# Kernel optimization log

Measured on AMD Instinct MI355X. Metric: run time of the kernel, lower is better.

Reference implementation:

```python
import jax, jax.numpy as jnp
import numpy as np

D_MODEL = 1024
N_HEADS = 16
HEAD_DIM = D_MODEL // N_HEADS


def setup_inputs() -> dict:
    key = jax.random.key(0)
    ks = jax.random.split(key, 5)
    B, T = 4, 4096
    x = jax.random.normal(ks[0], (B, T, D_MODEL), dtype=jnp.float32)
    s = 1.0 / np.sqrt(D_MODEL)
    Wqkv = jax.random.normal(ks[1], (D_MODEL, 3 * D_MODEL), dtype=jnp.float32) * s
    bqkv = jnp.zeros((3 * D_MODEL,), dtype=jnp.float32)
    Wout = jax.random.normal(ks[2], (D_MODEL, D_MODEL), dtype=jnp.float32) * s
    bout = jnp.zeros((D_MODEL,), dtype=jnp.float32)
    return {"x": x, "Wqkv": Wqkv, "bqkv": bqkv, "Wout": Wout, "bout": bout}


def _feature_map(x):
    # elu(x) + 1  (strictly positive feature map)
    return jax.nn.elu(x) + 1.0


def reference(x, Wqkv, bqkv, Wout, bout):
    B, T, C = x.shape
    H, D = N_HEADS, HEAD_DIM
    qkv = x @ Wqkv + bqkv                      # [B,T,3C]
    qkv = qkv.reshape(B, T, 3, H, D)
    qkv = jnp.transpose(qkv, (2, 0, 3, 1, 4))  # [3,B,H,T,D]
    q, k, v = qkv[0], qkv[1], qkv[2]
    scale = D ** 0.25
    q_m = _feature_map(q / scale)
    k_m = _feature_map(k / scale)
    kv = jnp.einsum('bhtd,bhtm->bhdm', k_m, v)     # [B,H,D,D]
    out = jnp.einsum('bhtd,bhdm->bhtm', q_m, kv)   # [B,H,T,D]
    z = q_m.sum(axis=-1, keepdims=True)            # note: sum over feature dim (as in source)
    out = out / (z + 1e-6)
    out = jnp.transpose(out, (0, 2, 1, 3)).reshape(B, T, C)
    return out @ Wout + bout
```

## Files before the change

kernel.cpp:

```cpp
#include <hip/hip_runtime.h>
#include <hip/hip_bf16.h>
#include <math.h>

#define B_ 4
#define T_ 4096
#define H_ 16
#define D_ 64
#define C_ 1024
#define BT_ (B_*T_)

using short8  = __attribute__((ext_vector_type(8))) short;
using floatx4 = __attribute__((ext_vector_type(4))) float;

__device__ __forceinline__ float feature_map(float x) {
    return x > 0.0f ? x + 1.0f : __expf(x);
}
__device__ __forceinline__ unsigned short f2bf(float x) {
    union { __hip_bfloat16 b; unsigned short u; } c;
    c.b = __float2bfloat16(x);
    return c.u;
}
__device__ __forceinline__ float bf2f(unsigned short u) {
    union { unsigned int u; float f; } c;
    c.u = (unsigned)u << 16;
    return c.f;
}
__device__ __forceinline__ void async16(const void* g, void* l) {
    __builtin_amdgcn_global_load_lds(
        (const __attribute__((address_space(1))) void*)g,
        (__attribute__((address_space(3))) void*)l, 16, 0, 0);
}

__global__ __launch_bounds__(256)
void convert_x_kernel(const float4* __restrict__ x, ushort* __restrict__ xb)
{
    const size_t i = (size_t)blockIdx.x * 256 + threadIdx.x;
    const float4 v = x[i];
    *reinterpret_cast<ushort4*>(&xb[i * 4]) =
        make_ushort4(f2bf(v.x), f2bf(v.y), f2bf(v.z), f2bf(v.w));
}

__global__ __launch_bounds__(256)
void transpose_bf16_kernel(const float* __restrict__ W, ushort* __restrict__ WT,
                           int K, int N)
{
    __shared__ float t[32][33];
    const int n0 = blockIdx.x * 32, k0 = blockIdx.y * 32;
    const int r = threadIdx.x >> 5, c = threadIdx.x & 31;
    #pragma unroll
    for (int i = 0; i < 4; i++)
        t[r + 8 * i][c] = W[(size_t)(k0 + r + 8 * i) * N + n0 + c];
    __syncthreads();
    #pragma unroll
    for (int i = 0; i < 4; i++)
        WT[(size_t)(n0 + r + 8 * i) * K + k0 + c] = f2bf(t[c][r + 8 * i]);
}

#define BAR()    __builtin_amdgcn_s_barrier()
#define WAITDS() do { asm volatile("s_waitcnt lgkmcnt(0)" ::: "memory"); \
                      __builtin_amdgcn_sched_barrier(0); } while(0)
#define VM6()    do { asm volatile("s_waitcnt vmcnt(6)" ::: "memory"); \
                      __builtin_amdgcn_sched_barrier(0); } while(0)

#define LDA(slot, mf, ks, buf) \
    aR[slot][ks] = *(const short8*)(smem + (buf)*32768 + ((mf)>>2)*16384 + \
                                    aRowB + ((mf)&3)*2048 + cks##ks)
#define LDB(nf, ks, buf) \
    bR[nf][ks] = *(const short8*)(smem + 65536 + (buf)*32768 + ((nf)>>1)*16384 + \
                                  bRowB + ((nf)&1)*2048 + cks##ks)
#define LDA8(MB, BUF) do { \
    LDA(0, MB+0, 0, BUF); LDA(0, MB+0, 1, BUF); \
    LDA(1, MB+1, 0, BUF); LDA(1, MB+1, 1, BUF); \
    LDA(2, MB+2, 0, BUF); LDA(2, MB+2, 1, BUF); \
    LDA(3, MB+3, 0, BUF); LDA(3, MB+3, 1, BUF); } while(0)
#define LDB4(NF, BUF) do { \
    LDB(NF+0, 0, BUF); LDB(NF+0, 1, BUF); \
    LDB(NF+1, 0, BUF); LDB(NF+1, 1, BUF); } while(0)

#define MM(mf, nf, ks, slot) \
    acc[mf][nf] = __builtin_amdgcn_mfma_f32_16x16x32_bf16( \
        aR[slot][ks], bR[nf][ks], acc[mf][nf], 0, 0, 0)
#define MFMAQ(MB, NF) do { \
    MM(MB+0,NF+0,0,0); MM(MB+1,NF+0,0,1); MM(MB+2,NF+0,0,2); MM(MB+3,NF+0,0,3); \
    MM(MB+0,NF+1,0,0); MM(MB+1,NF+1,0,1); MM(MB+2,NF+1,0,2); MM(MB+3,NF+1,0,3); \
    MM(MB+0,NF+0,1,0); MM(MB+1,NF+0,1,1); MM(MB+2,NF+0,1,2); MM(MB+3,NF+0,1,3); \
    MM(MB+0,NF+1,1,0); MM(MB+1,NF+1,1,1); MM(MB+2,NF+1,1,2); MM(MB+3,NF+1,1,3); \
} while(0)

#define STG(SRC, OPB, h, w, buf) do { \
    async16(SRC[h][0] + (size_t)(w)*128, \
            smem + (OPB) + (buf)*32768 + (h)*16384 + wv*1024); \
    async16(SRC[h][1] + (size_t)(w)*128, \
            smem + (OPB) + (buf)*32768 + (h)*16384 + 8192 + wv*1024); \
} while(0)

template<int EPI, int NBX>
__global__ __launch_bounds__(512, 2)
void gemm256_8ph(const ushort* __restrict__ A, const ushort* __restrict__ Bm,
                 const float* __restrict__ bias,
                 ushort* __restrict__ q_out, ushort* __restrict__ kT_out,
                 ushort* __restrict__ vT_out, float* __restrict__ f_out)
{
    __shared__ __align__(16) unsigned char smem[131072];

    const int tid = threadIdx.x;
    const int wv = tid >> 6, l = tid & 63;
    const int wm = wv >> 2, wn = wv & 3;
    const int lr = l & 15, quad = l >> 4;

    int wg = blockIdx.x;
    { const int cpx = (int)gridDim.x >> 3; wg = (wg & 7) * cpx + (wg >> 3); }
    const int mb = wg / NBX, nb = wg % NBX;
    const int mBase = mb * 256, nBase = nb * 256;

    const int s0 = tid >> 3;
    const int cb = ((tid & 7) * 16) ^ ((s0 & 7) << 4);
    const char* Abyte = (const char*)(A + (size_t)mBase * C_);
    const char* Bbyte = (const char*)(Bm + (size_t)nBase * C_);
    const char* aSrc[2][2]; const char* bSrc[2][2];
    #pragma unroll
    for (int h = 0; h < 2; h++) {
        aSrc[h][0] = Abyte + (size_t)(h * 64 + s0) * 2048 + cb;
        aSrc[h][1] = Abyte + (size_t)(128 + h * 64 + s0) * 2048 + cb;
        const int bq = (s0 >> 5) * 64 + h * 32 + (s0 & 31);
        bSrc[h][0] = Bbyte + (size_t)bq * 2048 + cb;
        bSrc[h][1] = Bbyte + (size_t)(bq + 128) * 2048 + cb;
    }

    const int aRowB = (wm * 64 + lr) * 128;
    const int bRowB = (wn * 32 + lr) * 128;
    const int cks0 = (quad * 16) ^ ((lr & 7) << 4);
    const int cks1 = 64 ^ cks0;

    floatx4 acc[8][4];
    #pragma unroll
    for (int i = 0; i < 8; i++)
        #pragma unroll
        for (int j = 0; j < 4; j++) acc[i][j] = (floatx4)0.0f;
    short8 aR[4][2], bR[4][2];

    STG(aSrc,     0, 0, 0, 0);
    STG(bSrc, 65536, 0, 0, 0);
    STG(bSrc, 65536, 1, 0, 0);
    STG(aSrc,     0, 1, 0, 0);
    STG(aSrc,     0, 0, 1, 1);
    STG(bSrc, 65536, 0, 1, 1);
    STG(bSrc, 65536, 1, 1, 1);
    asm volatile("s_waitcnt vmcnt(6)" ::: "memory");
    __builtin_amdgcn_sched_barrier(0);
    BAR();

    #pragma unroll 1
    for (int it = 0; it < 8; ++it) {
        const int t1v = 2 * it + 1;
        const int t2v = (2 * it + 2) & 15;
        const int t3v = (2 * it + 3) & 15;
        LDA8(0, 0); LDB4(0, 0);
        STG(aSrc, 0, 1, t1v, 1);
        BAR(); WAITDS(); __builtin_amdgcn_s_setprio(1); MFMAQ(0, 0);
        __builtin_amdgcn_s_setprio(0); BAR();
        LDB4(2, 0);
        STG(aSrc, 0, 0, t2v, 0);
        BAR(); WAITDS(); __builtin_amdgcn_s_setprio(1); MFMAQ(0, 2);
        __builtin_amdgcn_s_setprio(0); BAR();
        LDA8(4, 0);
        STG(bSrc, 65536, 0, t2v, 0);
        BAR(); WAITDS(); __builtin_amdgcn_s_setprio(1); MFMAQ(4, 2);
        __builtin_amdgcn_s_setprio(0); BAR();
        STG(bSrc, 65536, 1, t2v, 0);
        BAR(); WAITDS(); __builtin_amdgcn_s_setprio(1); MFMAQ(4, 0);
        __builtin_amdgcn_s_setprio(0); VM6(); BAR();
        LDA8(0, 1); LDB4(0, 1);
        STG(aSrc, 0, 1, t2v, 0);
        BAR(); WAITDS(); __builtin_amdgcn_s_setprio(1); MFMAQ(0, 0);
        __builtin_amdgcn_s_setprio(0); BAR();
        LDB4(2, 1);
        STG(aSrc, 0, 0, t3v, 1);
        BAR(); WAITDS(); __builtin_amdgcn_s_setprio(1); MFMAQ(0, 2);
        __builtin_amdgcn_s_setprio(0); BAR();
        LDA8(4, 1);
        STG(bSrc, 65536, 0, t3v, 1);
        BAR(); WAITDS(); __builtin_amdgcn_s_setprio(1); MFMAQ(4, 2);
        __builtin_amdgcn_s_setprio(0); BAR();
        STG(bSrc, 65536, 1, t3v, 1);
        BAR(); WAITDS(); __builtin_amdgcn_s_setprio(1); MFMAQ(4, 0);
        __builtin_amdgcn_s_setprio(0); VM6(); BAR();
    }

    if (EPI == 0) {
        const float inv_scale = 0.35355339059327373f;
        const int seg = nBase >> 10;
        if (seg == 0) {
            #pragma unroll
            for (int nf = 0; nf < 4; nf++) {
                const int c = nBase + wn * 64 + nf * 16 + lr;
                const float bv = bias[c];
                #pragma unroll
                for (int mf = 0; mf < 8; mf++)
                    #pragma unroll
                    for (int i = 0; i < 4; i++) {
                        const int t = mBase + wm * 128 + mf * 16 + quad * 4 + i;
                        q_out[(size_t)t * C_ + c] =
                            f2bf(feature_map((acc[mf][nf][i] + bv) * inv_scale));
                    }
            }
        } else {
            ushort* dstT = (seg == 1) ? kT_out : vT_out;
            #pragma unroll
            for (int nf = 0; nf < 4; nf++) {
                const int cfull = nBase + wn * 64 + nf * 16 + lr;
                const int c = cfull & 1023;
                const float bv = bias[cfull];
                #pragma unroll
                for (int mf = 0; mf < 8; mf++) {
                    float v0 = acc[mf][nf][0] + bv, v1 = acc[mf][nf][1] + bv;
                    float v2 = acc[mf][nf][2] + bv, v3 = acc[mf][nf][3] + bv;
                    if (seg == 1) {
                        v0 = feature_map(v0 * inv_scale); v1 = feature_map(v1 * inv_scale);
                        v2 = feature_map(v2 * inv_scale); v3 = feature_map(v3 * inv_scale);
                    }
                    const int tt = mBase + wm * 128 + mf * 16 + quad * 4;
                    *(ushort4*)&dstT[(size_t)c * BT_ + tt] =
                        make_ushort4(f2bf(v0), f2bf(v1), f2bf(v2), f2bf(v3));
                }
            }
        }
    } else {
        #pragma unroll
        for (int nf = 0; nf < 4; nf++) {
            const int c = nBase + wn * 64 + nf * 16 + lr;
            const float bv = bias[c];
            #pragma unroll
            for (int mf = 0; mf < 8; mf++)
                #pragma unroll
                for (int i = 0; i < 4; i++) {
                    const int row = mBase + wm * 128 + mf * 16 + quad * 4 + i;
                    f_out[(size_t)row * C_ + c] = acc[mf][nf][i] + bv;
                }
        }
    }
    asm volatile("s_waitcnt vmcnt(0)" ::: "memory");
}

__global__ __launch_bounds__(256)
void kv_accum_kernel(const ushort* __restrict__ kmT, const ushort* __restrict__ vT,
                     float* __restrict__ kv)
{
    const int tid = threadIdx.x;
    const int w = tid >> 6, l = tid & 63;
    const int wm = w >> 1, wn = w & 1;
    const int lr = l & 15, quad = l >> 4;
    const int bh = blockIdx.y;
    const int b = bh >> 4, h = bh & 15;
    const size_t t0 = (size_t)b * T_ + (size_t)blockIdx.x * 512;

    const ushort* Ar = kmT + (size_t)(h * 64 + wm * 32 + lr) * BT_ + t0 + quad * 8;
    const ushort* Br = vT  + (size_t)(h * 64 + wn * 32 + lr) * BT_ + t0 + quad * 8;

    floatx4 acc[2][2];
    #pragma unroll
    for (int i = 0; i < 2; i++)
        #pragma unroll
        for (int j = 0; j < 2; j++) acc[i][j] = (floatx4)0.0f;

    #pragma unroll 4
    for (int tt = 0; tt < 512; tt += 32) {
        const short8 af0 = *(const short8*)&Ar[tt];
        const short8 af1 = *(const short8*)&Ar[(size_t)16 * BT_ + tt];
        const short8 bf0 = *(const short8*)&Br[tt];
        const short8 bf1 = *(const short8*)&Br[(size_t)16 * BT_ + tt];
        acc[0][0] = __builtin_amdgcn_mfma_f32_16x16x32_bf16(af0, bf0, acc[0][0], 0, 0, 0);
        acc[0][1] = __builtin_amdgcn_mfma_f32_16x16x32_bf16(af0, bf1, acc[0][1], 0, 0, 0);
        acc[1][0] = __builtin_amdgcn_mfma_f32_16x16x32_bf16(af1, bf0, acc[1][0], 0, 0, 0);
        acc[1][1] = __builtin_amdgcn_mfma_f32_16x16x32_bf16(af1, bf1, acc[1][1], 0, 0, 0);
    }

    float* kvb = kv + (size_t)bh * (D_ * D_);
    #pragma unroll
    for (int i = 0; i < 2; i++)
        #pragma unroll
        for (int j = 0; j < 2; j++)
            #pragma unroll
            for (int r = 0; r < 4; r++) {
                const int d = wm * 32 + i * 16 + quad * 4 + r;
                const int m = wn * 32 + j * 16 + lr;
                atomicAdd(&kvb[d * 64 + m], acc[i][j][r]);
            }
}

__global__ __launch_bounds__(256)
void pv_kernel(const ushort* __restrict__ qm, const float* __restrict__ kv,
               ushort* __restrict__ attn)
{
    __shared__ ushort kvs[64 * 72];
    const int tid = threadIdx.x;
    const int w = tid >> 6, l = tid & 63;
    const int lr = l & 15, quad = l >> 4;
    const int h = blockIdx.x;
    const int tBase = blockIdx.y * 256;
    const int b = tBase >> 12;

    const float* kvg = kv + ((size_t)b * H_ + h) * (D_ * D_);
    #pragma unroll
    for (int e = 0; e < 4; e++) {
        const int flat = (e * 256 + tid) * 4;
        const float4 vv = *(const float4*)&kvg[flat];
        const int d = flat >> 6, m = flat & 63;
        kvs[(m + 0) * 72 + d] = f2bf(vv.x);
        kvs[(m + 1) * 72 + d] = f2bf(vv.y);
        kvs[(m + 2) * 72 + d] = f2bf(vv.z);
        kvs[(m + 3) * 72 + d] = f2bf(vv.w);
    }
    __syncthreads();

    const int tw = tBase + w * 64;

    floatx4 acc[4][4];
    #pragma unroll
    for (int i = 0; i < 4; i++)
        #pragma unroll
        for (int j = 0; j < 4; j++) acc[i][j] = (floatx4)0.0f;

    float zp[4] = {0.0f, 0.0f, 0.0f, 0.0f};

    #pragma unroll
    for (int kk = 0; kk < 2; kk++) {
        short8 bf[4];
        #pragma unroll
        for (int tf = 0; tf < 4; tf++) {
            bf[tf] = *(const short8*)&qm[(size_t)(tw + tf * 16 + lr) * C_
                                         + h * 64 + kk * 32 + quad * 8];
            #pragma unroll
            for (int j = 0; j < 8; j++) zp[tf] += bf2f((unsigned short)bf[tf][j]);
        }
        short8 af[4];
        #pragma unroll
        for (int mf = 0; mf < 4; mf++)
            af[mf] = *(const short8*)&kvs[(mf * 16 + lr) * 72 + kk * 32 + quad * 8];
        #pragma unroll
        for (int mf = 0; mf < 4; mf++)
            #pragma unroll
            for (int tf = 0; tf < 4; tf++)
                acc[mf][tf] = __builtin_amdgcn_mfma_f32_16x16x32_bf16(
                    af[mf], bf[tf], acc[mf][tf], 0, 0, 0);
    }

    #pragma unroll
    for (int tf = 0; tf < 4; tf++) {
        zp[tf] += __shfl_xor(zp[tf], 16);
        zp[tf] += __shfl_xor(zp[tf], 32);
    }

    #pragma unroll
    for (int tf = 0; tf < 4; tf++) {
        const int t = tw + tf * 16 + lr;
        const float inv = 1.0f / (zp[tf] + 1e-6f);
        #pragma unroll
        for (int mf = 0; mf < 4; mf++) {
            const int m = mf * 16 + quad * 4;
            *(ushort4*)&attn[(size_t)t * C_ + h * 64 + m] =
                make_ushort4(f2bf(acc[mf][tf][0] * inv), f2bf(acc[mf][tf][1] * inv),
                             f2bf(acc[mf][tf][2] * inv), f2bf(acc[mf][tf][3] * inv));
        }
    }
}

extern "C" void kernel_launch(void* const* d_in, const int* in_sizes, int n_in,
                              void* d_out, int out_size, void* d_ws, size_t ws_size,
                              hipStream_t stream)
{
    const float* x    = (const float*)d_in[0];
    const float* Wqkv = (const float*)d_in[1];
    const float* bqkv = (const float*)d_in[2];
    const float* Wout = (const float*)d_in[3];
    const float* bout = (const float*)d_in[4];
    float* out = (float*)d_out;

    char* ws = (char*)d_ws;
    ushort* xb     = (ushort*)ws;
    ushort* WqkvT  = (ushort*)(ws + 33554432);
    ushort* WoutT  = (ushort*)(ws + 39845888);
    ushort* vT     = (ushort*)(ws + 41943040);
    float*  kv     = (float*) (ws + 75497472);
    ushort* attn   = (ushort*)ws;
    ushort* qm     = (ushort*)d_out;
    ushort* kmT    = (ushort*)((char*)d_out + 33554432);

    hipMemsetAsync(kv, 0, (size_t)B_ * H_ * D_ * D_ * sizeof(float), stream);

    convert_x_kernel<<<(BT_ * C_ / 4) / 256, 256, 0, stream>>>((const float4*)x, xb);
    transpose_bf16_kernel<<<dim3(3 * C_ / 32, C_ / 32), 256, 0, stream>>>(Wqkv, WqkvT, C_, 3 * C_);
    transpose_bf16_kernel<<<dim3(C_ / 32, C_ / 32), 256, 0, stream>>>(Wout, WoutT, C_, C_);

    gemm256_8ph<0, 12><<<dim3(768), 512, 0, stream>>>(
        xb, WqkvT, bqkv, qm, kmT, vT, nullptr);
    kv_accum_kernel<<<dim3(8, B_ * H_), 256, 0, stream>>>(kmT, vT, kv);
    pv_kernel<<<dim3(H_, BT_ / 256), 256, 0, stream>>>(qm, kv, attn);
    gemm256_8ph<1, 4><<<dim3(256), 512, 0, stream>>>(
        attn, WoutT, bout, nullptr, nullptr, nullptr, out);
}
```

Measured before the change: 315.2 us.

## Make QKV GEMM persistent over three tiles with cross-tile prefetch

The QKV projection GEMM now launches 256 workgroups, and each computes three 256x256 output tiles in sequence. The global-to-LDS prefetch runs across tile boundaries, so loads for the next tile's first k-steps overlap the current tile's tail. Bias values are preloaded per tile and the epilogue is factored into a helper. This removes the pipeline prologue and drain for every tile after the first, at the cost of more registers, and the epilogue stores still stall between tiles. The x-to-bf16 conversion also handles 8 elements per thread with one 16-byte store, and the kv accumulation loop is unrolled further.

```diff
diff --git a/kernel.cpp b/kernel.cpp
--- a/kernel.cpp
+++ b/kernel.cpp
@@ -30,14 +30,22 @@
         (const __attribute__((address_space(1))) void*)g,
         (__attribute__((address_space(3))) void*)l, 16, 0, 0);
 }
+__device__ __forceinline__ const char* sel3(const char* a0, const char* a1,
+                                            const char* a2, int t) {
+    return t == 0 ? a0 : (t == 1 ? a1 : a2);
+}
 
 __global__ __launch_bounds__(256)
 void convert_x_kernel(const float4* __restrict__ x, ushort* __restrict__ xb)
 {
-    const size_t i = (size_t)blockIdx.x * 256 + threadIdx.x;
-    const float4 v = x[i];
-    *reinterpret_cast<ushort4*>(&xb[i * 4]) =
-        make_ushort4(f2bf(v.x), f2bf(v.y), f2bf(v.z), f2bf(v.w));
+    const size_t i = ((size_t)blockIdx.x * 256 + threadIdx.x) * 2;
+    const float4 a = x[i], b = x[i + 1];
+    short8 r;
+    r[0] = (short)f2bf(a.x); r[1] = (short)f2bf(a.y);
+    r[2] = (short)f2bf(a.z); r[3] = (short)f2bf(a.w);
+    r[4] = (short)f2bf(b.x); r[5] = (short)f2bf(b.y);
+    r[6] = (short)f2bf(b.z); r[7] = (short)f2bf(b.w);
+    *reinterpret_cast<short8*>(&xb[i * 4]) = r;
 }
 
 __global__ __launch_bounds__(256)
@@ -87,106 +95,51 @@
     MM(MB+0,NF+1,1,0); MM(MB+1,NF+1,1,1); MM(MB+2,NF+1,1,2); MM(MB+3,NF+1,1,3); \
 } while(0)
 
-#define STG(SRC, OPB, h, w, buf) do { \
-    async16(SRC[h][0] + (size_t)(w)*128, \
-            smem + (OPB) + (buf)*32768 + (h)*16384 + wv*1024); \
-    async16(SRC[h][1] + (size_t)(w)*128, \
-            smem + (OPB) + (buf)*32768 + (h)*16384 + 8192 + wv*1024); \
+#define STGA(h, G, buf) do { int _g = (G); if (_g >= NTILE*16) _g -= NTILE*16; \
+    const char* _b = sel3(Ab0, Ab1, Ab2, _g >> 4); const int _w = (_g & 15) * 128; \
+    async16(_b + aOf##h##0 + _w, smem + (buf)*32768 + (h)*16384 + wv*1024); \
+    async16(_b + aOf##h##1 + _w, smem + (buf)*32768 + (h)*16384 + 8192 + wv*1024); \
 } while(0)
-
-template<int EPI, int NBX>
-__global__ __launch_bounds__(512, 2)
-void gemm256_8ph(const ushort* __restrict__ A, const ushort* __restrict__ Bm,
-                 const float* __restrict__ bias,
-                 ushort* __restrict__ q_out, ushort* __restrict__ kT_out,
-                 ushort* __restrict__ vT_out, float* __restrict__ f_out)
-{
-    __shared__ __align__(16) unsigned char smem[131072];
-
-    const int tid = threadIdx.x;
-    const int wv = tid >> 6, l = tid & 63;
-    const int wm = wv >> 2, wn = wv & 3;
-    const int lr = l & 15, quad = l >> 4;
-
-    int wg = blockIdx.x;
-    { const int cpx = (int)gridDim.x >> 3; wg = (wg & 7) * cpx + (wg >> 3); }
-    const int mb = wg / NBX, nb = wg % NBX;
-    const int mBase = mb * 256, nBase = nb * 256;
-
-    const int s0 = tid >> 3;
-    const int cb = ((tid & 7) * 16) ^ ((s0 & 7) << 4);
-    const char* Abyte = (const char*)(A + (size_t)mBase * C_);
-    const char* Bbyte = (const char*)(Bm + (size_t)nBase * C_);
-    const char* aSrc[2][2]; const char* bSrc[2][2];
-    #pragma unroll
-    for (int h = 0; h < 2; h++) {
-        aSrc[h][0] = Abyte + (size_t)(h * 64 + s0) * 2048 + cb;
-        aSrc[h][1] = Abyte + (size_t)(128 + h * 64 + s0) * 2048 + cb;
-        const int bq = (s0 >> 5) * 64 + h * 32 + (s0 & 31);
-        bSrc[h][0] = Bbyte + (size_t)bq * 2048 + cb;
-        bSrc[h][1] = Bbyte + (size_t)(bq + 128) * 2048 + cb;
-    }
-
-    const int aRowB = (wm * 64 + lr) * 128;
-    const int bRowB = (wn * 32 + lr) * 128;
-    const int cks0 = (quad * 16) ^ ((lr & 7) << 4);
-    const int cks1 = 64 ^ cks0;
-
-    floatx4 acc[8][4];
-    #pragma unroll
-    for (int i = 0; i < 8; i++)
-        #pragma unroll
-        for (int j = 0; j < 4; j++) acc[i][j] = (floatx4)0.0f;
-    short8 aR[4][2], bR[4][2];
-
-    STG(aSrc,     0, 0, 0, 0);
-    STG(bSrc, 65536, 0, 0, 0);
-    STG(bSrc, 65536, 1, 0, 0);
-    STG(aSrc,     0, 1, 0, 0);
-    STG(aSrc,     0, 0, 1, 1);
-    STG(bSrc, 65536, 0, 1, 1);
-    STG(bSrc, 65536, 1, 1, 1);
-    asm volatile("s_waitcnt vmcnt(6)" ::: "memory");
-    __builtin_amdgcn_sched_barrier(0);
-    BAR();
-
-    #pragma unroll 1
-    for (int it = 0; it < 8; ++it) {
-        const int t1v = 2 * it + 1;
-        const int t2v = (2 * it + 2) & 15;
-        const int t3v = (2 * it + 3) & 15;
-        LDA8(0, 0); LDB4(0, 0);
-        STG(aSrc, 0, 1, t1v, 1);
-        BAR(); WAITDS(); __builtin_amdgcn_s_setprio(1); MFMAQ(0, 0);
-        __builtin_amdgcn_s_setprio(0); BAR();
-        LDB4(2, 0);
-        STG(aSrc, 0, 0, t2v, 0);
-        BAR(); WAITDS(); __builtin_amdgcn_s_setprio(1); MFMAQ(0, 2);
-        __builtin_amdgcn_s_setprio(0); BAR();
-        LDA8(4, 0);
-        STG(bSrc, 65536, 0, t2v, 0);
-        BAR(); WAITDS(); __builtin_amdgcn_s_setprio(1); MFMAQ(4, 2);
-        __builtin_amdgcn_s_setprio(0); BAR();
-        STG(bSrc, 65536, 1, t2v, 0);
-        BAR(); WAITDS(); __builtin_amdgcn_s_setprio(1); MFMAQ(4, 0);
-        __builtin_amdgcn_s_setprio(0); VM6(); BAR();
-        LDA8(0, 1); LDB4(0, 1);
-        STG(aSrc, 0, 1, t2v, 0);
-        BAR(); WAITDS(); __builtin_amdgcn_s_setprio(1); MFMAQ(0, 0);
-        __builtin_amdgcn_s_setprio(0); BAR();
-        LDB4(2, 1);
-        STG(aSrc, 0, 0, t3v, 1);
-        BAR(); WAITDS(); __builtin_amdgcn_s_setprio(1); MFMAQ(0, 2);
-        __builtin_amdgcn_s_setprio(0); BAR();
-        LDA8(4, 1);
-        STG(bSrc, 65536, 0, t3v, 1);
-        BAR(); WAITDS(); __builtin_amdgcn_s_setprio(1); MFMAQ(4, 2);
-        __builtin_amdgcn_s_setprio(0); BAR();
-        STG(bSrc, 65536, 1, t3v, 1);
-        BAR(); WAITDS(); __builtin_amdgcn_s_setprio(1); MFMAQ(4, 0);
-        __builtin_amdgcn_s_setprio(0); VM6(); BAR();
-    }
-
+#define STGB(h, G, buf) do { int _g = (G); if (_g >= NTILE*16) _g -= NTILE*16; \
+    const char* _b = sel3(Bb0, Bb1, Bb2, _g >> 4); const int _w = (_g & 15) * 128; \
+    async16(_b + bOf##h##0 + _w, smem + 65536 + (buf)*32768 + (h)*16384 + wv*1024); \
+    async16(_b + bOf##h##1 + _w, smem + 65536 + (buf)*32768 + (h)*16384 + 8192 + wv*1024); \
+} while(0)
+
+#define ITERBODY(GB) \
+    const int g1 = (GB) + 2*it + 1, g2 = (GB) + 2*it + 2, g3 = (GB) + 2*it + 3; \
+     LDA8(0, 0); LDB4(0, 0); STGA(1, g1, 1); \
+    BAR(); WAITDS(); __builtin_amdgcn_s_setprio(1); MFMAQ(0, 0); \
+    __builtin_amdgcn_s_setprio(0); BAR(); \
+     LDB4(2, 0); STGA(0, g2, 0); \
+    BAR(); WAITDS(); __builtin_amdgcn_s_setprio(1); MFMAQ(0, 2); \
+    __builtin_amdgcn_s_setprio(0); BAR(); \
+     LDA8(4, 0); STGB(0, g2, 0); \
+    BAR(); WAITDS(); __builtin_amdgcn_s_setprio(1); MFMAQ(4, 2); \
+    __builtin_amdgcn_s_setprio(0); BAR(); \
+     STGB(1, g2, 0); \
+    BAR(); WAITDS(); __builtin_amdgcn_s_setprio(1); MFMAQ(4, 0); \
+    __builtin_amdgcn_s_setprio(0); VM6(); BAR(); \
+     LDA8(0, 1); LDB4(0, 1); STGA(1, g2, 0); \
+    BAR(); WAITDS(); __builtin_amdgcn_s_setprio(1); MFMAQ(0, 0); \
+    __builtin_amdgcn_s_setprio(0); BAR(); \
+     LDB4(2, 1); STGA(0, g3, 1); \
+    BAR(); WAITDS(); __builtin_amdgcn_s_setprio(1); MFMAQ(0, 2); \
+    __builtin_amdgcn_s_setprio(0); BAR(); \
+     LDA8(4, 1); STGB(0, g3, 1); \
+    BAR(); WAITDS(); __builtin_amdgcn_s_setprio(1); MFMAQ(4, 2); \
+    __builtin_amdgcn_s_setprio(0); BAR(); \
+     STGB(1, g3, 1); \
+    BAR(); WAITDS(); __builtin_amdgcn_s_setprio(1); MFMAQ(4, 0); \
+    __builtin_amdgcn_s_setprio(0); VM6(); BAR();
+
+template<int EPI>
+__device__ __forceinline__ void gemm_epilogue(
+    floatx4 (&acc)[8][4], const float (&bv)[4],
+    int mBase, int nBase, int wm, int wn, int lr, int quad,
+    ushort* __restrict__ q_out, ushort* __restrict__ kT_out,
+    ushort* __restrict__ vT_out, float* __restrict__ f_out)
+{
     if (EPI == 0) {
         const float inv_scale = 0.35355339059327373f;
         const int seg = nBase >> 10;
@@ -194,27 +147,24 @@
             #pragma unroll
             for (int nf = 0; nf < 4; nf++) {
                 const int c = nBase + wn * 64 + nf * 16 + lr;
-                const float bv = bias[c];
                 #pragma unroll
                 for (int mf = 0; mf < 8; mf++)
                     #pragma unroll
                     for (int i = 0; i < 4; i++) {
                         const int t = mBase + wm * 128 + mf * 16 + quad * 4 + i;
                         q_out[(size_t)t * C_ + c] =
-                            f2bf(feature_map((acc[mf][nf][i] + bv) * inv_scale));
+                            f2bf(feature_map((acc[mf][nf][i] + bv[nf]) * inv_scale));
                     }
             }
         } else {
             ushort* dstT = (seg == 1) ? kT_out : vT_out;
             #pragma unroll
             for (int nf = 0; nf < 4; nf++) {
-                const int cfull = nBase + wn * 64 + nf * 16 + lr;
-                const int c = cfull & 1023;
-                const float bv = bias[cfull];
+                const int c = (nBase + wn * 64 + nf * 16 + lr) & 1023;
                 #pragma unroll
                 for (int mf = 0; mf < 8; mf++) {
-                    float v0 = acc[mf][nf][0] + bv, v1 = acc[mf][nf][1] + bv;
-                    float v2 = acc[mf][nf][2] + bv, v3 = acc[mf][nf][3] + bv;
+                    float v0 = acc[mf][nf][0] + bv[nf], v1 = acc[mf][nf][1] + bv[nf];
+                    float v2 = acc[mf][nf][2] + bv[nf], v3 = acc[mf][nf][3] + bv[nf];
                     if (seg == 1) {
                         v0 = feature_map(v0 * inv_scale); v1 = feature_map(v1 * inv_scale);
                         v2 = feature_map(v2 * inv_scale); v3 = feature_map(v3 * inv_scale);
@@ -229,15 +179,113 @@
         #pragma unroll
         for (int nf = 0; nf < 4; nf++) {
             const int c = nBase + wn * 64 + nf * 16 + lr;
-            const float bv = bias[c];
             #pragma unroll
             for (int mf = 0; mf < 8; mf++)
                 #pragma unroll
                 for (int i = 0; i < 4; i++) {
                     const int row = mBase + wm * 128 + mf * 16 + quad * 4 + i;
-                    f_out[(size_t)row * C_ + c] = acc[mf][nf][i] + bv;
+                    f_out[(size_t)row * C_ + c] = acc[mf][nf][i] + bv[nf];
                 }
         }
+    }
+    #pragma unroll
+    for (int i = 0; i < 8; i++)
+        #pragma unroll
+        for (int j = 0; j < 4; j++) acc[i][j] = (floatx4)0.0f;
+}
+
+template<int EPI, int NBX, int NTILE>
+__global__ __launch_bounds__(512, 2)
+void gemm256_8ph(const ushort* __restrict__ A, const ushort* __restrict__ Bm,
+                 const float* __restrict__ bias,
+                 ushort* __restrict__ q_out, ushort* __restrict__ kT_out,
+                 ushort* __restrict__ vT_out, float* __restrict__ f_out)
+{
+    __shared__ __align__(16) unsigned char smem[131072];
+
+    const int tid = threadIdx.x;
+    const int wv = tid >> 6, l = tid & 63;
+    const int wm = wv >> 2, wn = wv & 3;
+    const int lr = l & 15, quad = l >> 4;
+
+    int mB0, mB1, mB2, nB0, nB1, nB2;
+    {
+        const int tot = (int)gridDim.x * NTILE, cpx = tot >> 3;
+        int lg0 = blockIdx.x;
+        int w0 = (lg0 & 7) * cpx + (lg0 >> 3);
+        mB0 = (w0 / NBX) * 256; nB0 = (w0 % NBX) * 256;
+        if (NTILE > 1) {
+            int lg1 = blockIdx.x + (int)gridDim.x;
+            int w1 = (lg1 & 7) * cpx + (lg1 >> 3);
+            mB1 = (w1 / NBX) * 256; nB1 = (w1 % NBX) * 256;
+            int lg2 = blockIdx.x + 2 * (int)gridDim.x;
+            int w2 = (lg2 & 7) * cpx + (lg2 >> 3);
+            mB2 = (w2 / NBX) * 256; nB2 = (w2 % NBX) * 256;
+        } else { mB1 = mB0; nB1 = nB0; mB2 = mB0; nB2 = nB0; }
+    }
+    const char* Ab0 = (const char*)(A + (size_t)mB0 * C_);
+    const char* Ab1 = (const char*)(A + (size_t)mB1 * C_);
+    const char* Ab2 = (const char*)(A + (size_t)mB2 * C_);
+    const char* Bb0 = (const char*)(Bm + (size_t)nB0 * C_);
+    const char* Bb1 = (const char*)(Bm + (size_t)nB1 * C_);
+    const char* Bb2 = (const char*)(Bm + (size_t)nB2 * C_);
+
+    float bv0[4], bv1[4], bv2[4];
+    #pragma unroll
+    for (int nf = 0; nf < 4; nf++) {
+        bv0[nf] = bias[nB0 + wn * 64 + nf * 16 + lr];
+        bv1[nf] = (NTILE > 1) ? bias[nB1 + wn * 64 + nf * 16 + lr] : bv0[nf];
+        bv2[nf] = (NTILE > 1) ? bias[nB2 + wn * 64 + nf * 16 + lr] : bv0[nf];
+    }
+
+    const int s0 = tid >> 3;
+    const int cb = ((tid & 7) * 16) ^ ((s0 & 7) << 4);
+    const int aOf00 = (s0)       * 2048 + cb;
+    const int aOf01 = (128 + s0) * 2048 + cb;
+    const int aOf10 = (64 + s0)  * 2048 + cb;
+    const int aOf11 = (192 + s0) * 2048 + cb;
+    const int bq    = (s0 >> 5) * 64 + (s0 & 31);
+    const int bOf00 = (bq)       * 2048 + cb;
+    const int bOf01 = (bq + 128) * 2048 + cb;
+    const int bOf10 = (bq + 32)  * 2048 + cb;
+    const int bOf11 = (bq + 160) * 2048 + cb;
+
+    const int aRowB = (wm * 64 + lr) * 128;
+    const int bRowB = (wn * 32 + lr) * 128;
+    const int cks0 = (quad * 16) ^ ((lr & 7) << 4);
+    const int cks1 = 64 ^ cks0;
+
+    floatx4 acc[8][4];
+    #pragma unroll
+    for (int i = 0; i < 8; i++)
+        #pragma unroll
+        for (int j = 0; j < 4; j++) acc[i][j] = (floatx4)0.0f;
+    short8 aR[4][2], bR[4][2];
+
+    STGA(0, 0, 0);
+    STGB(0, 0, 0);
+    STGB(1, 0, 0);
+    STGA(1, 0, 0);
+    STGA(0, 1, 1);
+    STGB(0, 1, 1);
+    STGB(1, 1, 1);
+    asm volatile("s_waitcnt vmcnt(6)" ::: "memory");
+    __builtin_amdgcn_sched_barrier(0);
+    BAR();
+
+    #pragma unroll 1
+    for (int it = 0; it < 8; ++it) { ITERBODY(0) }
+    gemm_epilogue<EPI>(acc, bv0, mB0, nB0, wm, wn, lr, quad,
+                       q_out, kT_out, vT_out, f_out);
+    if (NTILE > 1) {
+        #pragma unroll 1
+        for (int it = 0; it < 8; ++it) { ITERBODY(16) }
+        gemm_epilogue<EPI>(acc, bv1, mB1, nB1, wm, wn, lr, quad,
+                           q_out, kT_out, vT_out, f_out);
+        #pragma unroll 1
+        for (int it = 0; it < 8; ++it) { ITERBODY(32) }
+        gemm_epilogue<EPI>(acc, bv2, mB2, nB2, wm, wn, lr, quad,
+                           q_out, kT_out, vT_out, f_out);
     }
     asm volatile("s_waitcnt vmcnt(0)" ::: "memory");
 }
@@ -263,7 +311,7 @@
         #pragma unroll
         for (int j = 0; j < 2; j++) acc[i][j] = (floatx4)0.0f;
 
-    #pragma unroll 4
+    #pragma unroll 8
     for (int tt = 0; tt < 512; tt += 32) {
         const short8 af0 = *(const short8*)&Ar[tt];
         const short8 af1 = *(const short8*)&Ar[(size_t)16 * BT_ + tt];
@@ -388,14 +436,14 @@
 
     hipMemsetAsync(kv, 0, (size_t)B_ * H_ * D_ * D_ * sizeof(float), stream);
 
-    convert_x_kernel<<<(BT_ * C_ / 4) / 256, 256, 0, stream>>>((const float4*)x, xb);
+    convert_x_kernel<<<(BT_ * C_ / 8) / 256, 256, 0, stream>>>((const float4*)x, xb);
     transpose_bf16_kernel<<<dim3(3 * C_ / 32, C_ / 32), 256, 0, stream>>>(Wqkv, WqkvT, C_, 3 * C_);
     transpose_bf16_kernel<<<dim3(C_ / 32, C_ / 32), 256, 0, stream>>>(Wout, WoutT, C_, C_);
 
-    gemm256_8ph<0, 12><<<dim3(768), 512, 0, stream>>>(
+    gemm256_8ph<0, 12, 3><<<dim3(256), 512, 0, stream>>>(
         xb, WqkvT, bqkv, qm, kmT, vT, nullptr);
     kv_accum_kernel<<<dim3(8, B_ * H_), 256, 0, stream>>>(kmT, vT, kv);
     pv_kernel<<<dim3(H_, BT_ / 256), 256, 0, stream>>>(qm, kv, attn);
-    gemm256_8ph<1, 4><<<dim3(256), 512, 0, stream>>>(
+    gemm256_8ph<1, 4, 1><<<dim3(256), 512, 0, stream>>>(
         attn, WoutT, bout, nullptr, nullptr, nullptr, out);
 }
```

Result: no change. 312.1 us (-1.0%).
